# Performance work log

Hardware: AMD Instinct MI355X
Metric: run time of the kernel (lower is better)

Reference implementation:

```python
import jax, jax.numpy as jnp
import numpy as np

DIM = 512
H = 256
W = 256
N = 32768


def _dwconv(x, w, b):
    # x: [1, C, W, H], w: [C, 1, k, k] depthwise, b: [C]
    y = jax.lax.conv_general_dilated(
        x, w, window_strides=(1, 1), padding='SAME',
        feature_group_count=w.shape[0],
        dimension_numbers=('NCHW', 'OIHW', 'NCHW'))
    return y + b[None, :, None, None]


def setup_inputs() -> dict:
    rng = np.random.default_rng(0)
    # unique, lexicographically sorted occupied cells; force corners so
    # grid extent after pos - pos.min() is exactly H x W
    inner = rng.choice(H * W - 2, size=N - 2, replace=False) + 1
    idx = np.sort(np.concatenate([[0], inner, [H * W - 1]])).astype(np.int32)
    pos = np.stack([idx // W, idx % W], axis=1)  # [N, 2]

    key = jax.random.key(0)
    ks = jax.random.split(key, 7)
    x = jax.random.normal(ks[0], (1, N, DIM), jnp.float32)
    w1 = jax.random.normal(ks[1], (DIM, 1, 3, 3), jnp.float32) * 0.05
    b1 = jax.random.normal(ks[2], (DIM,), jnp.float32) * 0.05
    w2 = jax.random.normal(ks[3], (DIM, 1, 5, 5), jnp.float32) * 0.05
    b2 = jax.random.normal(ks[4], (DIM,), jnp.float32) * 0.05
    w3 = jax.random.normal(ks[5], (DIM, 1, 7, 7), jnp.float32) * 0.05
    b3 = jax.random.normal(ks[6], (DIM,), jnp.float32) * 0.05
    return {'x': x, 'pos': jnp.asarray(pos), 'w1': w1, 'b1': b1,
            'w2': w2, 'b2': b2, 'w3': w3, 'b3': b3}


def reference(x, pos, w1, b1, w2, b2, w3, b3):
    pos = pos - pos.min(axis=0)            # shift to origin
    vals = x[0]                            # [N, DIM]
    # scatter points onto dense grid (duplicate coords sum, like coalesce)
    dense = jnp.zeros((H, W, DIM), x.dtype).at[pos[:, 0], pos[:, 1]].add(vals)
    # permute(2,1,0).unsqueeze(0): [H,W,DIM] -> [1, DIM, W, H]
    x_dense = dense.transpose(2, 1, 0)[None]
    x_pos = _dwconv(x_dense, w1, b1) + _dwconv(x_dense, w2, b2) + _dwconv(x_dense, w3, b3)
    mask = x_dense.sum(axis=1) != 0.0      # [1, W, H] occupied cells
    x_pos = jnp.where(mask[:, None], x_pos, 0.0) + x_dense
    # squeeze().permute(2,1,0) -> [H, W, DIM]; to_sparse(2).values() gathers
    # occupied cells in lexicographic (h, w) order == input pos order here
    grid = x_pos[0].transpose(2, 1, 0)
    out = grid[pos[:, 0], pos[:, 1]][None]  # [1, N, DIM]
    return out
```

## Files before the change

### kernel.cpp

```cpp
#include <hip/hip_runtime.h>

#define DIM 512
#define H 256
#define W 256

__global__ __launch_bounds__(512) void prep_kernel(
    const int* __restrict__ pos, int n,
    const float* __restrict__ k3, const float* __restrict__ b1,
    const float* __restrict__ k5, const float* __restrict__ b2,
    const float* __restrict__ k7, const float* __restrict__ b3,
    float* __restrict__ weff, float* __restrict__ bsum,
    int* __restrict__ map) {
    int b = blockIdx.x;
    if (b < 49) {
        int o = b;
        int c = threadIdx.x;
        int dh = o / 7 - 3, dw = o % 7 - 3;
        float v = k7[c * 49 + (dw + 3) * 7 + (dh + 3)];
        if (dh >= -2 && dh <= 2 && dw >= -2 && dw <= 2)
            v += k5[c * 25 + (dw + 2) * 5 + (dh + 2)];
        if (dh >= -1 && dh <= 1 && dw >= -1 && dw <= 1)
            v += k3[c * 9 + (dw + 1) * 3 + (dh + 1)];
        weff[o * DIM + c] = v;
        if (o == 0) bsum[c] = b1[c] + b2[c] + b3[c];
    } else {
        int i = (b - 49) * 512 + threadIdx.x;
        if (i < n) {
            int h = pos[2 * i], w = pos[2 * i + 1];
            map[h * W + w] = i;
        }
    }
}

__global__ __launch_bounds__(128) void gather_conv_kernel(
    const float* __restrict__ x, const int* __restrict__ pos,
    const int* __restrict__ map, const float* __restrict__ weff,
    const float* __restrict__ bsum, float* __restrict__ out, int n) {
    int bid = blockIdx.x;
    int i = ((n & 7) == 0) ? ((bid & 7) * (n >> 3) + (bid >> 3)) : bid;
    int tid = threadIdx.x;

    __shared__ int s_list[49];
    __shared__ int s_cnt;
    if (tid == 0) s_cnt = 0;
    __syncthreads();

    int h = pos[2 * i], w = pos[2 * i + 1];
    if (tid < 49) {
        int dh = tid / 7 - 3, dw = tid % 7 - 3;
        int hh = h + dh, ww = w + dw;
        if (hh >= 0 && hh < H && ww >= 0 && ww < W) {
            int j = map[hh * W + ww];
            if ((unsigned)j < (unsigned)n && pos[2 * j] == hh && pos[2 * j + 1] == ww) {
                int slot = atomicAdd(&s_cnt, 1);
                s_list[slot] = (j << 6) | tid;
            }
        }
    }
    __syncthreads();

    int c = tid * 4;
    float4 acc = *(const float4*)(x + (size_t)i * DIM + c);
    float4 bb  = *(const float4*)(bsum + c);
    acc.x += bb.x; acc.y += bb.y; acc.z += bb.z; acc.w += bb.w;

    int cnt = s_cnt;
    int k = 0;
    for (; k + 4 <= cnt; k += 4) {
        int p0 = s_list[k + 0], p1 = s_list[k + 1];
        int p2 = s_list[k + 2], p3 = s_list[k + 3];
        float4 w0 = *(const float4*)(weff + (p0 & 63) * DIM + c);
        float4 x0 = *(const float4*)(x + (size_t)(p0 >> 6) * DIM + c);
        float4 w1 = *(const float4*)(weff + (p1 & 63) * DIM + c);
        float4 x1 = *(const float4*)(x + (size_t)(p1 >> 6) * DIM + c);
        float4 w2 = *(const float4*)(weff + (p2 & 63) * DIM + c);
        float4 x2 = *(const float4*)(x + (size_t)(p2 >> 6) * DIM + c);
        float4 w3 = *(const float4*)(weff + (p3 & 63) * DIM + c);
        float4 x3 = *(const float4*)(x + (size_t)(p3 >> 6) * DIM + c);
        acc.x = fmaf(w0.x, x0.x, acc.x);
        acc.y = fmaf(w0.y, x0.y, acc.y);
        acc.z = fmaf(w0.z, x0.z, acc.z);
        acc.w = fmaf(w0.w, x0.w, acc.w);
        acc.x = fmaf(w1.x, x1.x, acc.x);
        acc.y = fmaf(w1.y, x1.y, acc.y);
        acc.z = fmaf(w1.z, x1.z, acc.z);
        acc.w = fmaf(w1.w, x1.w, acc.w);
        acc.x = fmaf(w2.x, x2.x, acc.x);
        acc.y = fmaf(w2.y, x2.y, acc.y);
        acc.z = fmaf(w2.z, x2.z, acc.z);
        acc.w = fmaf(w2.w, x2.w, acc.w);
        acc.x = fmaf(w3.x, x3.x, acc.x);
        acc.y = fmaf(w3.y, x3.y, acc.y);
        acc.z = fmaf(w3.z, x3.z, acc.z);
        acc.w = fmaf(w3.w, x3.w, acc.w);
    }
    for (; k < cnt; ++k) {
        int pk = s_list[k];
        float4 wv = *(const float4*)(weff + (pk & 63) * DIM + c);
        float4 xv = *(const float4*)(x + (size_t)(pk >> 6) * DIM + c);
        acc.x = fmaf(wv.x, xv.x, acc.x);
        acc.y = fmaf(wv.y, xv.y, acc.y);
        acc.z = fmaf(wv.z, xv.z, acc.z);
        acc.w = fmaf(wv.w, xv.w, acc.w);
    }
    *(float4*)(out + (size_t)i * DIM + c) = acc;
}

extern "C" void kernel_launch(void* const* d_in, const int* in_sizes, int n_in,
                              void* d_out, int out_size, void* d_ws, size_t ws_size,
                              hipStream_t stream) {
    const float* x   = (const float*)d_in[0];
    const int*   pos = (const int*)d_in[1];
    const float* k3  = (const float*)d_in[2];
    const float* b1  = (const float*)d_in[3];
    const float* k5  = (const float*)d_in[4];
    const float* b2  = (const float*)d_in[5];
    const float* k7  = (const float*)d_in[6];
    const float* b3  = (const float*)d_in[7];
    float* out = (float*)d_out;

    char* ws = (char*)d_ws;
    int*   map  = (int*)ws;
    float* weff = (float*)(ws + (size_t)H * W * 4);
    float* bsum = (float*)(ws + (size_t)H * W * 4 + 49 * DIM * 4);

    int n = in_sizes[1] / 2;

    int scatter_blocks = (n + 511) / 512;
    prep_kernel<<<49 + scatter_blocks, 512, 0, stream>>>(
        pos, n, k3, b1, k5, b2, k7, b3, weff, bsum, map);
    gather_conv_kernel<<<n, 128, 0, stream>>>(x, pos, map, weff, bsum, out, n);
}
```

Baseline: 227.1 us.

## Process two points per block with one wavefront each, 8 channels per lane

After: 230.9 us. No clear change (+1.7%).

```diff
diff --git a/kernel.cpp b/kernel.cpp
--- a/kernel.cpp
+++ b/kernel.cpp
@@ -33,77 +33,92 @@
 }
 
 __global__ __launch_bounds__(128) void gather_conv_kernel(
-    const float* __restrict__ x, const int* __restrict__ pos,
+    const float* __restrict__ x, const int2* __restrict__ pos2,
     const int* __restrict__ map, const float* __restrict__ weff,
     const float* __restrict__ bsum, float* __restrict__ out, int n) {
-    int bid = blockIdx.x;
-    int i = ((n & 7) == 0) ? ((bid & 7) * (n >> 3) + (bid >> 3)) : bid;
-    int tid = threadIdx.x;
+    int g = blockIdx.x;
+    int ng = gridDim.x;
+    int gs = ((ng & 7) == 0) ? ((g & 7) * (ng >> 3) + (g >> 3)) : g;
+    int wv = threadIdx.x >> 6;
+    int lane = threadIdx.x & 63;
+    int i = gs * 2 + wv;
+    bool valid = (i < n);
 
-    __shared__ int s_list[49];
-    __shared__ int s_cnt;
-    if (tid == 0) s_cnt = 0;
+    __shared__ int s_list[2][49];
+    __shared__ int s_cnt[2];
+    if (lane == 0) s_cnt[wv] = 0;
     __syncthreads();
 
-    int h = pos[2 * i], w = pos[2 * i + 1];
-    if (tid < 49) {
-        int dh = tid / 7 - 3, dw = tid % 7 - 3;
-        int hh = h + dh, ww = w + dw;
+    if (valid && lane < 49) {
+        int2 pw = pos2[i];
+        int dh = lane / 7 - 3, dw = lane % 7 - 3;
+        int hh = pw.x + dh, ww = pw.y + dw;
         if (hh >= 0 && hh < H && ww >= 0 && ww < W) {
             int j = map[hh * W + ww];
-            if ((unsigned)j < (unsigned)n && pos[2 * j] == hh && pos[2 * j + 1] == ww) {
-                int slot = atomicAdd(&s_cnt, 1);
-                s_list[slot] = (j << 6) | tid;
+            if ((unsigned)j < (unsigned)n) {
+                int2 pj = pos2[j];
+                if (pj.x == hh && pj.y == ww) {
+                    int slot = atomicAdd(&s_cnt[wv], 1);
+                    s_list[wv][slot] = (j << 6) | lane;
+                }
             }
         }
     }
     __syncthreads();
 
-    int c = tid * 4;
-    float4 acc = *(const float4*)(x + (size_t)i * DIM + c);
-    float4 bb  = *(const float4*)(bsum + c);
-    acc.x += bb.x; acc.y += bb.y; acc.z += bb.z; acc.w += bb.w;
+    if (!valid) return;
 
-    int cnt = s_cnt;
-    int k = 0;
-    for (; k + 4 <= cnt; k += 4) {
-        int p0 = s_list[k + 0], p1 = s_list[k + 1];
-        int p2 = s_list[k + 2], p3 = s_list[k + 3];
-        float4 w0 = *(const float4*)(weff + (p0 & 63) * DIM + c);
-        float4 x0 = *(const float4*)(x + (size_t)(p0 >> 6) * DIM + c);
-        float4 w1 = *(const float4*)(weff + (p1 & 63) * DIM + c);
-        float4 x1 = *(const float4*)(x + (size_t)(p1 >> 6) * DIM + c);
-        float4 w2 = *(const float4*)(weff + (p2 & 63) * DIM + c);
-        float4 x2 = *(const float4*)(x + (size_t)(p2 >> 6) * DIM + c);
-        float4 w3 = *(const float4*)(weff + (p3 & 63) * DIM + c);
-        float4 x3 = *(const float4*)(x + (size_t)(p3 >> 6) * DIM + c);
-        acc.x = fmaf(w0.x, x0.x, acc.x);
-        acc.y = fmaf(w0.y, x0.y, acc.y);
-        acc.z = fmaf(w0.z, x0.z, acc.z);
-        acc.w = fmaf(w0.w, x0.w, acc.w);
-        acc.x = fmaf(w1.x, x1.x, acc.x);
-        acc.y = fmaf(w1.y, x1.y, acc.y);
-        acc.z = fmaf(w1.z, x1.z, acc.z);
-        acc.w = fmaf(w1.w, x1.w, acc.w);
-        acc.x = fmaf(w2.x, x2.x, acc.x);
-        acc.y = fmaf(w2.y, x2.y, acc.y);
-        acc.z = fmaf(w2.z, x2.z, acc.z);
-        acc.w = fmaf(w2.w, x2.w, acc.w);
-        acc.x = fmaf(w3.x, x3.x, acc.x);
-        acc.y = fmaf(w3.y, x3.y, acc.y);
-        acc.z = fmaf(w3.z, x3.z, acc.z);
-        acc.w = fmaf(w3.w, x3.w, acc.w);
+    int c = lane * 8;
+    const float* xi = x + (size_t)i * DIM + c;
+    float4 acc0 = *(const float4*)(xi);
+    float4 acc1 = *(const float4*)(xi + 4);
+    float4 b0 = *(const float4*)(bsum + c);
+    float4 b1 = *(const float4*)(bsum + c + 4);
+    acc0.x += b0.x; acc0.y += b0.y; acc0.z += b0.z; acc0.w += b0.w;
+    acc1.x += b1.x; acc1.y += b1.y; acc1.z += b1.z; acc1.w += b1.w;
+
+    int cnt = s_cnt[wv];
+    const int* lst = s_list[wv];
+
+    if (cnt > 0) {
+        int pk = lst[0];
+        const float* wp = weff + (pk & 63) * DIM + c;
+        const float* xp = x + (size_t)(pk >> 6) * DIM + c;
+        float4 wa0 = *(const float4*)(wp);
+        float4 wa1 = *(const float4*)(wp + 4);
+        float4 xa0 = *(const float4*)(xp);
+        float4 xa1 = *(const float4*)(xp + 4);
+        for (int k = 1; k < cnt; ++k) {
+            int pk2 = lst[k];
+            const float* wp2 = weff + (pk2 & 63) * DIM + c;
+            const float* xp2 = x + (size_t)(pk2 >> 6) * DIM + c;
+            float4 wb0 = *(const float4*)(wp2);
+            float4 wb1 = *(const float4*)(wp2 + 4);
+            float4 xb0 = *(const float4*)(xp2);
+            float4 xb1 = *(const float4*)(xp2 + 4);
+            acc0.x = fmaf(wa0.x, xa0.x, acc0.x);
+            acc0.y = fmaf(wa0.y, xa0.y, acc0.y);
+            acc0.z = fmaf(wa0.z, xa0.z, acc0.z);
+            acc0.w = fmaf(wa0.w, xa0.w, acc0.w);
+            acc1.x = fmaf(wa1.x, xa1.x, acc1.x);
+            acc1.y = fmaf(wa1.y, xa1.y, acc1.y);
+            acc1.z = fmaf(wa1.z, xa1.z, acc1.z);
+            acc1.w = fmaf(wa1.w, xa1.w, acc1.w);
+            wa0 = wb0; wa1 = wb1; xa0 = xb0; xa1 = xb1;
+        }
+        acc0.x = fmaf(wa0.x, xa0.x, acc0.x);
+        acc0.y = fmaf(wa0.y, xa0.y, acc0.y);
+        acc0.z = fmaf(wa0.z, xa0.z, acc0.z);
+        acc0.w = fmaf(wa0.w, xa0.w, acc0.w);
+        acc1.x = fmaf(wa1.x, xa1.x, acc1.x);
+        acc1.y = fmaf(wa1.y, xa1.y, acc1.y);
+        acc1.z = fmaf(wa1.z, xa1.z, acc1.z);
+        acc1.w = fmaf(wa1.w, xa1.w, acc1.w);
     }
-    for (; k < cnt; ++k) {
-        int pk = s_list[k];
-        float4 wv = *(const float4*)(weff + (pk & 63) * DIM + c);
-        float4 xv = *(const float4*)(x + (size_t)(pk >> 6) * DIM + c);
-        acc.x = fmaf(wv.x, xv.x, acc.x);
-        acc.y = fmaf(wv.y, xv.y, acc.y);
-        acc.z = fmaf(wv.z, xv.z, acc.z);
-        acc.w = fmaf(wv.w, xv.w, acc.w);
-    }
-    *(float4*)(out + (size_t)i * DIM + c) = acc;
+
+    float* op = out + (size_t)i * DIM + c;
+    *(float4*)(op) = acc0;
+    *(float4*)(op + 4) = acc1;
 }
 
 extern "C" void kernel_launch(void* const* d_in, const int* in_sizes, int n_in,
@@ -129,5 +144,7 @@
     int scatter_blocks = (n + 511) / 512;
     prep_kernel<<<49 + scatter_blocks, 512, 0, stream>>>(
         pos, n, k3, b1, k5, b2, k7, b3, weff, bsum, map);
-    gather_conv_kernel<<<n, 128, 0, stream>>>(x, pos, map, weff, bsum, out, n);
+    int ngroups = (n + 1) / 2;
+    gather_conv_kernel<<<ngroups, 128, 0, stream>>>(
+        x, (const int2*)pos, map, weff, bsum, out, n);
 }
```

## Replace per-point gather conv with dense 8x8 spatial tiles using shared-memory halo

Applied to the files above, without the earlier changes.

Measured after the change: 459.0 us. 102% more time.

```diff
diff --git a/kernel.cpp b/kernel.cpp
--- a/kernel.cpp
+++ b/kernel.cpp
@@ -3,6 +3,11 @@
 #define DIM 512
 #define H 256
 #define W 256
+#define TS 8
+#define HS 14
+#define NH (HS * HS)
+#define CG 64
+#define NTX (W / TS)
 
 __global__ __launch_bounds__(512) void prep_kernel(
     const int* __restrict__ pos, int n,
@@ -32,78 +37,84 @@
     }
 }
 
-__global__ __launch_bounds__(128) void gather_conv_kernel(
-    const float* __restrict__ x, const int* __restrict__ pos,
+__global__ __launch_bounds__(256, 3) void tile_conv_kernel(
+    const float* __restrict__ x, const int2* __restrict__ pos2,
     const int* __restrict__ map, const float* __restrict__ weff,
     const float* __restrict__ bsum, float* __restrict__ out, int n) {
+
+    __shared__ float xs[NH][CG];
+    __shared__ int s_j[TS * TS];
+
     int bid = blockIdx.x;
-    int i = ((n & 7) == 0) ? ((bid & 7) * (n >> 3) + (bid >> 3)) : bid;
+    int cg = bid & 7;
+    int tile = bid >> 3;
+    int ty = tile >> 5, tx = tile & (NTX - 1);
+    int th0 = ty * TS, tw0 = tx * TS;
+
     int tid = threadIdx.x;
+    int wv = tid >> 6, lane = tid & 63;
+    int cbase = cg * CG + lane;
 
-    __shared__ int s_list[49];
-    __shared__ int s_cnt;
-    if (tid == 0) s_cnt = 0;
-    __syncthreads();
+    float wr[49];
+    #pragma unroll
+    for (int o = 0; o < 49; ++o) wr[o] = weff[o * DIM + cbase];
+    float bs = bsum[cbase];
 
-    int h = pos[2 * i], w = pos[2 * i + 1];
-    if (tid < 49) {
-        int dh = tid / 7 - 3, dw = tid % 7 - 3;
-        int hh = h + dh, ww = w + dw;
-        if (hh >= 0 && hh < H && ww >= 0 && ww < W) {
-            int j = map[hh * W + ww];
-            if ((unsigned)j < (unsigned)n && pos[2 * j] == hh && pos[2 * j + 1] == ww) {
-                int slot = atomicAdd(&s_cnt, 1);
-                s_list[slot] = (j << 6) | tid;
+    for (int hc = wv; hc < NH; hc += 4) {
+        int hy = hc / HS, hx = hc % HS;
+        int gh = th0 - 3 + hy, gw = tw0 - 3 + hx;
+        int j = -1;
+        if (gh >= 0 && gh < H && gw >= 0 && gw < W) {
+            int jj = map[gh * W + gw];
+            if ((unsigned)jj < (unsigned)n) {
+                int2 pj = pos2[jj];
+                if (pj.x == gh && pj.y == gw) j = jj;
             }
         }
+        float xv = (j >= 0) ? x[(size_t)j * DIM + cbase] : 0.0f;
+        xs[hc][lane] = xv;
+        if (lane == 0 && hy >= 3 && hy < 3 + TS && hx >= 3 && hx < 3 + TS)
+            s_j[(hy - 3) * TS + (hx - 3)] = j;
     }
     __syncthreads();
 
-    int c = tid * 4;
-    float4 acc = *(const float4*)(x + (size_t)i * DIM + c);
-    float4 bb  = *(const float4*)(bsum + c);
-    acc.x += bb.x; acc.y += bb.y; acc.z += bb.z; acc.w += bb.w;
+    int r0 = wv * 2;
+    float acc0[TS], acc1[TS];
+    #pragma unroll
+    for (int cx = 0; cx < TS; ++cx) { acc0[cx] = 0.0f; acc1[cx] = 0.0f; }
 
-    int cnt = s_cnt;
-    int k = 0;
-    for (; k + 4 <= cnt; k += 4) {
-        int p0 = s_list[k + 0], p1 = s_list[k + 1];
-        int p2 = s_list[k + 2], p3 = s_list[k + 3];
-        float4 w0 = *(const float4*)(weff + (p0 & 63) * DIM + c);
-        float4 x0 = *(const float4*)(x + (size_t)(p0 >> 6) * DIM + c);
-        float4 w1 = *(const float4*)(weff + (p1 & 63) * DIM + c);
-        float4 x1 = *(const float4*)(x + (size_t)(p1 >> 6) * DIM + c);
-        float4 w2 = *(const float4*)(weff + (p2 & 63) * DIM + c);
-        float4 x2 = *(const float4*)(x + (size_t)(p2 >> 6) * DIM + c);
-        float4 w3 = *(const float4*)(weff + (p3 & 63) * DIM + c);
-        float4 x3 = *(const float4*)(x + (size_t)(p3 >> 6) * DIM + c);
-        acc.x = fmaf(w0.x, x0.x, acc.x);
-        acc.y = fmaf(w0.y, x0.y, acc.y);
-        acc.z = fmaf(w0.z, x0.z, acc.z);
-        acc.w = fmaf(w0.w, x0.w, acc.w);
-        acc.x = fmaf(w1.x, x1.x, acc.x);
-        acc.y = fmaf(w1.y, x1.y, acc.y);
-        acc.z = fmaf(w1.z, x1.z, acc.z);
-        acc.w = fmaf(w1.w, x1.w, acc.w);
-        acc.x = fmaf(w2.x, x2.x, acc.x);
-        acc.y = fmaf(w2.y, x2.y, acc.y);
-        acc.z = fmaf(w2.z, x2.z, acc.z);
-        acc.w = fmaf(w2.w, x2.w, acc.w);
-        acc.x = fmaf(w3.x, x3.x, acc.x);
-        acc.y = fmaf(w3.y, x3.y, acc.y);
-        acc.z = fmaf(w3.z, x3.z, acc.z);
-        acc.w = fmaf(w3.w, x3.w, acc.w);
+    #pragma unroll
+    for (int t = 0; t < 8; ++t) {
+        float xr[HS];
+        #pragma unroll
+        for (int m = 0; m < HS; ++m) xr[m] = xs[(r0 + t) * HS + m][lane];
+        if (t < 7) {
+            #pragma unroll
+            for (int v = 0; v < 7; ++v)
+                #pragma unroll
+                for (int cx = 0; cx < TS; ++cx)
+                    acc0[cx] = fmaf(wr[t * 7 + v], xr[cx + v], acc0[cx]);
+        }
+        if (t >= 1) {
+            #pragma unroll
+            for (int v = 0; v < 7; ++v)
+                #pragma unroll
+                for (int cx = 0; cx < TS; ++cx)
+                    acc1[cx] = fmaf(wr[(t - 1) * 7 + v], xr[cx + v], acc1[cx]);
+        }
     }
-    for (; k < cnt; ++k) {
-        int pk = s_list[k];
-        float4 wv = *(const float4*)(weff + (pk & 63) * DIM + c);
-        float4 xv = *(const float4*)(x + (size_t)(pk >> 6) * DIM + c);
-        acc.x = fmaf(wv.x, xv.x, acc.x);
-        acc.y = fmaf(wv.y, xv.y, acc.y);
-        acc.z = fmaf(wv.z, xv.z, acc.z);
-        acc.w = fmaf(wv.w, xv.w, acc.w);
+
+    #pragma unroll
+    for (int cx = 0; cx < TS; ++cx) {
+        int j0 = s_j[r0 * TS + cx];
+        if (j0 >= 0)
+            out[(size_t)j0 * DIM + cbase] =
+                acc0[cx] + xs[(r0 + 3) * HS + (cx + 3)][lane] + bs;
+        int j1 = s_j[(r0 + 1) * TS + cx];
+        if (j1 >= 0)
+            out[(size_t)j1 * DIM + cbase] =
+                acc1[cx] + xs[(r0 + 4) * HS + (cx + 3)][lane] + bs;
     }
-    *(float4*)(out + (size_t)i * DIM + c) = acc;
 }
 
 extern "C" void kernel_launch(void* const* d_in, const int* in_sizes, int n_in,
@@ -129,5 +140,9 @@
     int scatter_blocks = (n + 511) / 512;
     prep_kernel<<<49 + scatter_blocks, 512, 0, stream>>>(
         pos, n, k3, b1, k5, b2, k7, b3, weff, bsum, map);
-    gather_conv_kernel<<<n, 128, 0, stream>>>(x, pos, map, weff, bsum, out, n);
+
+    int ntiles = (H / TS) * (W / TS);
+    int nblocks = ntiles * (DIM / CG);
+    tile_conv_kernel<<<nblocks, 256, 0, stream>>>(
+        x, (const int2*)pos, map, weff, bsum, out, n);
 }
```
